# Performance work log

Hardware: AMD Instinct MI355X
Metric: run time of the kernel (lower is better)

The kernel has to match this reference:

```python
import jax, jax.numpy as jnp
import numpy as np

B, T, H, OUT = 16384, 128, 256, 10
EPS = 1e-5


def setup_inputs() -> dict:
    key = jax.random.key(0)
    ks = jax.random.split(key, 8)
    x = jax.random.randint(ks[0], (B, T, 1), 0, 10).astype(jnp.float32)
    def lin(k, fan_out, fan_in):
        bound = 1.0 / np.sqrt(fan_in)
        kw, kb = jax.random.split(k)
        w = jax.random.uniform(kw, (fan_out, fan_in), jnp.float32, -bound, bound)
        b = jax.random.uniform(kb, (fan_out,), jnp.float32, -bound, bound)
        return w, b
    embed_w, embed_b = lin(ks[1], H, 1)
    update_w, update_b = lin(ks[2], H, H)
    out_w, out_b = lin(ks[3], OUT, H)
    return {
        "x": x,
        "embed_w": embed_w, "embed_b": embed_b,
        "update_w": update_w, "update_b": update_b,
        "gamma": jnp.ones((H,), jnp.float32), "beta": jnp.zeros((H,), jnp.float32),
        "out_w": out_w, "out_b": out_b,
    }


def _layer_norm(h, gamma, beta):
    mu = jnp.mean(h, axis=-1, keepdims=True)
    var = jnp.mean(jnp.square(h - mu), axis=-1, keepdims=True)
    return (h - mu) * jax.lax.rsqrt(var + EPS) * gamma + beta


def reference(x, embed_w, embed_b, update_w, update_b, gamma, beta, out_w, out_b):
    # embed is per-timestep independent -> precompute for all T at once: [B,T,H]
    inp_all = jnp.tanh(jnp.einsum('bti,hi->bth', x, embed_w) + embed_b)

    def step(h, inp_t):  # h:[B,H], inp_t:[B,H]
        h = jnp.tanh((inp_t + h) @ update_w.T + update_b)
        h = _layer_norm(h, gamma, beta)
        return h, None

    h0 = jnp.zeros((x.shape[0], embed_w.shape[0]), x.dtype)
    h, _ = jax.lax.scan(step, h0, jnp.swapaxes(inp_all, 0, 1))  # scan over T
    return h @ out_w.T + out_b  # [B, 10]
```

## Files before the change

kernel.cpp:

```cpp
#include <hip/hip_runtime.h>
#include <hip/hip_fp16.h>
#include <math.h>

typedef _Float16 f16;
typedef _Float16 f16x2 __attribute__((ext_vector_type(2)));
typedef _Float16 f16x8 __attribute__((ext_vector_type(8)));
typedef float f32x4 __attribute__((ext_vector_type(4)));
typedef unsigned char u8;

#define HDIM 256
#define TST 128
#define OUTD 10
#define S2LE 2.8853900817779268f

static __device__ __forceinline__ f16x2 pkrtz(float a, float b) {
  auto r = __builtin_amdgcn_cvt_pkrtz(a, b);
  return *(f16x2*)&r;
}

__global__ __launch_bounds__(256, 2) void rnn_kernel(
    const float* __restrict__ x,
    const float* __restrict__ embed_w,
    const float* __restrict__ embed_b,
    const float* __restrict__ update_w,
    const float* __restrict__ update_b,
    const float* __restrict__ gamma,
    const float* __restrict__ beta,
    const float* __restrict__ out_w,
    const float* __restrict__ out_b,
    float* __restrict__ out)
{
  __shared__ __align__(16) f16   sFR[2][8][64][8];
  __shared__ __align__(16) float sD1[10 * 260];
  __shared__ __align__(16) float sBW[HDIM];
  __shared__ __align__(16) float sRSg[HDIM];
  __shared__ __align__(16) float sST[2][16][10][2];
  __shared__ float sOB[16];
  __shared__ u8    sXb[TST][32];

  const int tid = threadIdx.x;
  const int w  = tid >> 6;
  const int l  = tid & 63;
  const int q  = l >> 4;
  const int ml = l & 15;
  const int m3 = ml & 3;
  const int base = blockIdx.x * 32;
  const int nb = w * 64 + q * 4;
  const int diagw = (q == (ml >> 2));

  float* T0 = (float*)&sFR[0][0][0][0];

  {
    float ew = embed_w[tid], eb = embed_b[tid];
    #pragma unroll
    for (int xv = 0; xv < 10; xv++)
      T0[tid * 10 + xv] = tanhf((float)xv * ew + eb);
  }
  for (int idx = tid; idx < 32 * TST; idx += 256) {
    int col = idx >> 7, tt = idx & 127;
    sXb[tt][col] = (u8)(int)x[(size_t)(base + col) * TST + tt];
  }
  if (tid < 16) {
    float v = 0.f;
    if (tid < OUTD) {
      v = out_b[tid];
      const float* orow = out_w + tid * HDIM;
      for (int k = 0; k < HDIM; k += 4) {
        float4 wv = *(const float4*)(orow + k);
        float4 bv = *(const float4*)(beta + k);
        v = fmaf(wv.x, bv.x, fmaf(wv.y, bv.y, fmaf(wv.z, bv.z, fmaf(wv.w, bv.w, v))));
      }
    }
    sOB[tid] = v;
  }
  __syncthreads();

  {
    const int n = tid;
    const float* wrow = update_w + n * HDIM;
    float ty[10];
    #pragma unroll
    for (int xv = 0; xv < 10; xv++) ty[xv] = 0.f;
    float bw = 0.f, rsg = 0.f;
    for (int k = 0; k < HDIM; k += 4) {
      float4 wv4 = *(const float4*)(wrow + k);
      float4 b4  = *(const float4*)(beta + k);
      float4 g4  = *(const float4*)(gamma + k);
      bw  = fmaf(wv4.x, b4.x, fmaf(wv4.y, b4.y, fmaf(wv4.z, b4.z, fmaf(wv4.w, b4.w, bw))));
      rsg = fmaf(wv4.x, S2LE * g4.x, fmaf(wv4.y, S2LE * g4.y,
            fmaf(wv4.z, S2LE * g4.z, fmaf(wv4.w, S2LE * g4.w, rsg))));
      #pragma unroll
      for (int kk = 0; kk < 4; kk++) {
        float wv = ((const float*)&wv4)[kk];
        const float* t0r = T0 + (k + kk) * 10;
        #pragma unroll
        for (int xv = 0; xv < 10; xv++) ty[xv] = fmaf(wv, t0r[xv], ty[xv]);
      }
    }
    float ubn = update_b[n];
    sBW[n]  = S2LE * bw;
    sRSg[n] = rsg;
    #pragma unroll
    for (int xv = 0; xv < 10; xv++)
      sD1[xv * 260 + n] = S2LE * (ty[xv] + ubn + bw);
  }
  __syncthreads();

  f16x8 wf[4][8];
  #pragma unroll
  for (int c = 0; c < 8; c++) {
    const int k0 = c * 32 + q * 4;
    float4 g0 = *(const float4*)(gamma + k0);
    float4 g1 = *(const float4*)(gamma + k0 + 16);
    #pragma unroll
    for (int nt = 0; nt < 4; nt++) {
      const float* wrow = update_w + (w * 64 + nt * 16 + ml) * HDIM;
      float4 a0 = *(const float4*)(wrow + k0);
      float4 a1 = *(const float4*)(wrow + k0 + 16);
      f16x8 f;
      f[0]=(f16)(S2LE*g0.x*a0.x); f[1]=(f16)(S2LE*g0.y*a0.y);
      f[2]=(f16)(S2LE*g0.z*a0.z); f[3]=(f16)(S2LE*g0.w*a0.w);
      f[4]=(f16)(S2LE*g1.x*a1.x); f[5]=(f16)(S2LE*g1.y*a1.y);
      f[6]=(f16)(S2LE*g1.z*a1.z); f[7]=(f16)(S2LE*g1.w*a1.w);
      wf[nt][c] = f;
    }
  }
  f32x4 rsgr[4];
  #pragma unroll
  for (int nt = 0; nt < 4; nt++)
    rsgr[nt] = *(const f32x4*)(sRSg + nb + nt * 16);

  f16x8 ones_;
  #pragma unroll
  for (int j = 0; j < 8; j++) ones_[j] = (f16)1.f;
  const f32x4 zeros_ = {0.f, 0.f, 0.f, 0.f};

  f32x4 acc0[4], acc1[4];

  {
    #pragma unroll
    for (int g = 0; g < 2; g++) {
      const int xv0 = (int)sXb[0][g * 16 + ml];
      const float* dp = sD1 + xv0 * 260;
      #pragma unroll
      for (int cp = 0; cp < 2; cp++) {
        union { f16x8 v8; f16x2 v2[4]; } pk;
        #pragma unroll
        for (int h = 0; h < 2; h++) {
          const int nt = 2 * cp + h;
          f32x4 dd = *(const f32x4*)(dp + nb + nt * 16);
          f32x4 bw = *(const f32x4*)(sBW + nb + nt * 16);
          float tq[4];
          #pragma unroll
          for (int r = 0; r < 4; r++) {
            float y = dd[r] - bw[r];
            float e = __builtin_amdgcn_exp2f(y);
            float tv = fmaf(-2.f, __builtin_amdgcn_rcpf(e + 1.f), 1.f);
            tq[r] = tv;
          }
          pk.v2[2 * h]     = pkrtz(tq[0], tq[1]);
          pk.v2[2 * h + 1] = pkrtz(tq[2], tq[3]);
        }
        *(f16x8*)&sFR[g][2 * w + cp][l][0] = pk.v8;
      }
    }
    __syncthreads();
  }

#define MMG(FB, CC, CUR, NXT, ACC)                                             \
    { if ((CC) < 7) NXT = *(const f16x8*)((FB) + ((CC) + 1) * 512 + l * 8);    \
      ACC[0] = __builtin_amdgcn_mfma_f32_16x16x32_f16(wf[0][CC], CUR, ACC[0],0,0,0); \
      ACC[1] = __builtin_amdgcn_mfma_f32_16x16x32_f16(wf[1][CC], CUR, ACC[1],0,0,0); \
      ACC[2] = __builtin_amdgcn_mfma_f32_16x16x32_f16(wf[2][CC], CUR, ACC[2],0,0,0); \
      ACC[3] = __builtin_amdgcn_mfma_f32_16x16x32_f16(wf[3][CC], CUR, ACC[3],0,0,0); }

#define GSEL(AG, SEL)                                                          \
    { SEL = AG[0];                                                             \
      SEL = (m3 == 1) ? AG[1] : SEL;                                           \
      SEL = (m3 == 2) ? AG[2] : SEL;                                           \
      SEL = (m3 == 3) ? AG[3] : SEL; }

#define STATRD(G, S1, S2)                                                      \
    { const float* sp_ = &sST[G][ml][0][0];                                    \
      f32x4 a0_ = *(const f32x4*)(sp_);                                        \
      f32x4 a1_ = *(const f32x4*)(sp_ + 4);                                    \
      f32x4 a2_ = *(const f32x4*)(sp_ + 8);                                    \
      f32x4 a3_ = *(const f32x4*)(sp_ + 12);                                   \
      S1 = ((a0_[0] + a0_[2]) + (a1_[0] + a1_[2]))                             \
         + ((a2_[0] + a2_[2]) + (a3_[0] + a3_[2]));                            \
      S2 = ((a0_[1] + a0_[3]) + (a1_[1] + a1_[3]))                             \
         + ((a2_[1] + a2_[3]) + (a3_[1] + a3_[3])); }

#define STATOWN(FB, G)                                                         \
    { f16x8 ro0_ = *(const f16x8*)((FB) + (2 * w) * 512 + l * 8);              \
      f16x8 ro1_ = *(const f16x8*)((FB) + (2 * w + 1) * 512 + l * 8);          \
      f32x4 aG0_ = __builtin_amdgcn_mfma_f32_16x16x32_f16(ro0_, ro0_, zeros_,0,0,0); \
      f32x4 aS0_ = __builtin_amdgcn_mfma_f32_16x16x32_f16(ones_, ro0_, zeros_,0,0,0); \
      f32x4 aG1_ = __builtin_amdgcn_mfma_f32_16x16x32_f16(ro1_, ro1_, zeros_,0,0,0); \
      f32x4 aS1_ = __builtin_amdgcn_mfma_f32_16x16x32_f16(ones_, ro1_, zeros_,0,0,0); \
      float sel0_, sel1_;                                                      \
      GSEL(aG0_, sel0_)                                                        \
      GSEL(aG1_, sel1_)                                                        \
      if (diagw)                                                               \
        *(f32x4*)&sST[G][ml][2 * w][0] =                                       \
            (f32x4){aS0_[0], sel0_, aS1_[0], sel1_};                           \
    }

#define SLICE(S, ACCE)                                                         \
    { _Pragma("unroll") for (int r_ = 0; r_ < 4; r_++) {                       \
        float y_ = fmaf(rs_, ACCE[S][r_], fmaf(-rm_, rsgr[S][r_], dd_[S][r_]));\
        float e_ = __builtin_amdgcn_exp2f(y_);                                 \
        tv_[S][r_] = fmaf(-2.f, __builtin_amdgcn_rcpf(e_ + 1.f), 1.f); } }

#define PACK(GE, CP)                                                           \
    { union { f16x8 v8; f16x2 v2[4]; } k_;                                     \
      k_.v2[0] = pkrtz(tv_[2*(CP)][0],   tv_[2*(CP)][1]);                      \
      k_.v2[1] = pkrtz(tv_[2*(CP)][2],   tv_[2*(CP)][3]);                      \
      k_.v2[2] = pkrtz(tv_[2*(CP)+1][0], tv_[2*(CP)+1][1]);                    \
      k_.v2[3] = pkrtz(tv_[2*(CP)+1][2], tv_[2*(CP)+1][3]);                    \
      *(f16x8*)&sFR[GE][2 * w + (CP)][l][0] = k_.v8; }

#define PHASE(TE, GM, GE, XOFF, ACCM, ACCE)                                    \
  {                                                                            \
    float s1_, s2_;                                                            \
    STATRD(GE, s1_, s2_)                                                       \
    const int xv_ = (int)sXb[TE][XOFF + ml];                                   \
    const float* dp_ = sD1 + xv_ * 260 + nb;                                   \
    f32x4 dd_[4];                                                              \
    _Pragma("unroll") for (int n_ = 0; n_ < 4; n_++)                           \
      dd_[n_] = *(const f32x4*)(dp_ + n_ * 16);                                \
    const f16* fbm_ = &sFR[GM][0][0][0];                                       \
    f16x8 rA_ = *(const f16x8*)(fbm_ + l * 8);                                 \
    f16x8 rB_;                                                                 \
    f32x4 tv_[4];                                                              \
    __builtin_amdgcn_s_setprio(1);                                             \
    rB_ = *(const f16x8*)(fbm_ + 512 + l * 8);                                 \
    ACCM[0] = __builtin_amdgcn_mfma_f32_16x16x32_f16(wf[0][0], rA_, zeros_,0,0,0); \
    ACCM[1] = __builtin_amdgcn_mfma_f32_16x16x32_f16(wf[1][0], rA_, zeros_,0,0,0); \
    ACCM[2] = __builtin_amdgcn_mfma_f32_16x16x32_f16(wf[2][0], rA_, zeros_,0,0,0); \
    ACCM[3] = __builtin_amdgcn_mfma_f32_16x16x32_f16(wf[3][0], rA_, zeros_,0,0,0); \
    MMG(fbm_, 1, rB_, rA_, ACCM)                                               \
    float mu_ = s1_ * (1.f / 256.f);                                           \
    float rs_ = __frsqrt_rn(fmaf(s2_, 1.f / 256.f, -mu_ * mu_) + 1e-5f);       \
    float rm_ = rs_ * mu_;                                                     \
    SLICE(0, ACCE)                                                             \
    MMG(fbm_, 2, rA_, rB_, ACCM)                                               \
    MMG(fbm_, 3, rB_, rA_, ACCM)                                               \
    SLICE(1, ACCE)                                                             \
    PACK(GE, 0)                                                                \
    MMG(fbm_, 4, rA_, rB_, ACCM)                                               \
    MMG(fbm_, 5, rB_, rA_, ACCM)                                               \
    SLICE(2, ACCE)                                                             \
    MMG(fbm_, 6, rA_, rB_, ACCM)                                               \
    MMG(fbm_, 7, rB_, rA_, ACCM)                                               \
    SLICE(3, ACCE)                                                             \
    PACK(GE, 1)                                                                \
    STATOWN(fbm_, GM)                                                          \
    __builtin_amdgcn_s_setprio(0);                                             \
    __syncthreads();                                                           \
  }

  {
    const f16* fbm_ = &sFR[0][0][0][0];
    f16x8 rA_ = *(const f16x8*)(fbm_ + l * 8);
    f16x8 rB_;
    rB_ = *(const f16x8*)(fbm_ + 512 + l * 8);
    acc0[0] = __builtin_amdgcn_mfma_f32_16x16x32_f16(wf[0][0], rA_, zeros_,0,0,0);
    acc0[1] = __builtin_amdgcn_mfma_f32_16x16x32_f16(wf[1][0], rA_, zeros_,0,0,0);
    acc0[2] = __builtin_amdgcn_mfma_f32_16x16x32_f16(wf[2][0], rA_, zeros_,0,0,0);
    acc0[3] = __builtin_amdgcn_mfma_f32_16x16x32_f16(wf[3][0], rA_, zeros_,0,0,0);
    MMG(fbm_, 1, rB_, rA_, acc0)
    MMG(fbm_, 2, rA_, rB_, acc0)
    MMG(fbm_, 3, rB_, rA_, acc0)
    MMG(fbm_, 4, rA_, rB_, acc0)
    MMG(fbm_, 5, rB_, rA_, acc0)
    MMG(fbm_, 6, rA_, rB_, acc0)
    MMG(fbm_, 7, rB_, rA_, acc0)
    STATOWN(fbm_, 0)
    __syncthreads();
  }

  #pragma unroll 1
  for (int t = 1; t <= 127; t++) {
    PHASE(t, 1, 0, 0,  acc1, acc0)
    PHASE(t, 0, 1, 16, acc0, acc1)
  }

  {
    const f16* fb1 = &sFR[1][0][0][0];
    STATOWN(fb1, 1)
    f16x8 fin0[2], fin1[2];
    #pragma unroll
    for (int cp = 0; cp < 2; cp++) {
      fin0[cp] = *(const f16x8*)&sFR[0][2 * w + cp][l][0];
      fin1[cp] = *(const f16x8*)&sFR[1][2 * w + cp][l][0];
    }
    __syncthreads();

    float rsF[2], nmF[2];
    {
      float s1, s2;
      STATRD(0, s1, s2)
      float mu = s1 * (1.f / 256.f);
      float ve = fmaf(s2, 1.f / 256.f, -mu * mu) + 1e-5f;
      rsF[0] = __frsqrt_rn(ve); nmF[0] = -rsF[0] * mu;
      STATRD(1, s1, s2)
      mu = s1 * (1.f / 256.f);
      ve = fmaf(s2, 1.f / 256.f, -mu * mu) + 1e-5f;
      rsF[1] = __frsqrt_rn(ve); nmF[1] = -rsF[1] * mu;
    }

    f16* sOW = (f16*)sD1;
    for (int idx = tid; idx < 512; idx += 256) {
      int c = idx >> 6, l2 = idx & 63, q2 = l2 >> 4, o = l2 & 15;
      int k0 = c * 32 + q2 * 4;
      f16x8 f;
      #pragma unroll
      for (int j = 0; j < 8; j++) f[j] = (f16)0.f;
      if (o < OUTD) {
        const float* orow = out_w + o * HDIM;
        float4 a0 = *(const float4*)(orow + k0);
        float4 a1 = *(const float4*)(orow + k0 + 16);
        float4 g0 = *(const float4*)(gamma + k0);
        float4 g1 = *(const float4*)(gamma + k0 + 16);
        f[0]=(f16)(g0.x*a0.x); f[1]=(f16)(g0.y*a0.y); f[2]=(f16)(g0.z*a0.z); f[3]=(f16)(g0.w*a0.w);
        f[4]=(f16)(g1.x*a1.x); f[5]=(f16)(g1.y*a1.y); f[6]=(f16)(g1.z*a1.z); f[7]=(f16)(g1.w*a1.w);
      }
      *(f16x8*)(sOW + idx * 8) = f;
    }
    __syncthreads();

    float* sOut = (float*)&sFR[0][0][0][0];
    #pragma unroll
    for (int g = 0; g < 2; g++) {
      f32x4 aO = zeros_;
      #pragma unroll
      for (int cp = 0; cp < 2; cp++) {
        f16x8 fr = (g == 0) ? fin0[cp] : fin1[cp];
        f16x8 af;
        #pragma unroll
        for (int j = 0; j < 8; j++)
          af[j] = (f16)fmaf(rsF[g], (float)fr[j], nmF[g]);
        f16x8 of = *(const f16x8*)(sOW + ((size_t)(2 * w + cp) * 64 + l) * 8);
        aO = __builtin_amdgcn_mfma_f32_16x16x32_f16(of, af, aO, 0, 0, 0);
      }
      #pragma unroll
      for (int r = 0; r < 4; r++)
        sOut[((g * 4 + w) * 16 + ml) * 16 + q * 4 + r] = aO[r];
    }
    __syncthreads();
    for (int idx = tid; idx < 32 * OUTD; idx += 256) {
      int m = idx / OUTD, o = idx - m * OUTD;
      int g = m >> 4, mm = m & 15;
      float s = 0.f;
      #pragma unroll
      for (int ww = 0; ww < 4; ww++) s += sOut[((g * 4 + ww) * 16 + mm) * 16 + o];
      out[(size_t)(base + m) * OUTD + o] = s + sOB[o];
    }
  }
}

extern "C" void kernel_launch(void* const* d_in, const int* in_sizes, int n_in,
                              void* d_out, int out_size, void* d_ws, size_t ws_size,
                              hipStream_t stream) {
  const float* x   = (const float*)d_in[0];
  const float* ew  = (const float*)d_in[1];
  const float* eb  = (const float*)d_in[2];
  const float* uw  = (const float*)d_in[3];
  const float* ub  = (const float*)d_in[4];
  const float* g   = (const float*)d_in[5];
  const float* be  = (const float*)d_in[6];
  const float* ow  = (const float*)d_in[7];
  const float* ob  = (const float*)d_in[8];
  float* out = (float*)d_out;

  const int B = in_sizes[0] / TST;
  const int grid = B / 32;
  hipLaunchKernelGGL(rnn_kernel, dim3(grid), dim3(256), 0, stream,
                     x, ew, eb, uw, ub, g, be, ow, ob, out);
}
```

Measured before the change: 317.9 us.

## Prefetch next-step embed rows and hoist LN stat MFMAs to phase start

The per-phase embedding lookup (sD1 rows indexed by the next timestep's token) is now loaded one phase ahead into persistent ddA/ddB registers, so it leaves the critical path. The Gram/sum MFMAs that feed layer-norm statistics are issued at the start of each phase rather than at the end, and their reduction and store move to the tail. The s_setprio hints are removed and the last iteration is peeled out. This costs extra VGPRs for the prefetched rows and the early stat results, which may push register pressure against the 2-wave launch bound.

```diff
diff --git a/kernel.cpp b/kernel.cpp
--- a/kernel.cpp
+++ b/kernel.cpp
@@ -136,6 +136,7 @@
   const f32x4 zeros_ = {0.f, 0.f, 0.f, 0.f};
 
   f32x4 acc0[4], acc1[4];
+  f32x4 ddA[4], ddB[4];
 
   {
     #pragma unroll
@@ -206,9 +207,9 @@
             (f32x4){aS0_[0], sel0_, aS1_[0], sel1_};                           \
     }
 
-#define SLICE(S, ACCE)                                                         \
+#define SLICE(S, ACCE, DD)                                                     \
     { _Pragma("unroll") for (int r_ = 0; r_ < 4; r_++) {                       \
-        float y_ = fmaf(rs_, ACCE[S][r_], fmaf(-rm_, rsgr[S][r_], dd_[S][r_]));\
+        float y_ = fmaf(rs_, ACCE[S][r_], fmaf(-rm_, rsgr[S][r_], DD[S][r_])); \
         float e_ = __builtin_amdgcn_exp2f(y_);                                 \
         tv_[S][r_] = fmaf(-2.f, __builtin_amdgcn_rcpf(e_ + 1.f), 1.f); } }
 
@@ -220,20 +221,20 @@
       k_.v2[3] = pkrtz(tv_[2*(CP)+1][2], tv_[2*(CP)+1][3]);                    \
       *(f16x8*)&sFR[GE][2 * w + (CP)][l][0] = k_.v8; }
 
-#define PHASE(TE, GM, GE, XOFF, ACCM, ACCE)                                    \
+#define PHASE(TE, TN, GM, GE, XOFF, ACCM, ACCE, DD)                            \
   {                                                                            \
+    const f16* fbm_ = &sFR[GM][0][0][0];                                       \
+    f16x8 ro0_ = *(const f16x8*)(fbm_ + (2 * w) * 512 + l * 8);                \
+    f16x8 ro1_ = *(const f16x8*)(fbm_ + (2 * w + 1) * 512 + l * 8);            \
+    f32x4 aG0_ = __builtin_amdgcn_mfma_f32_16x16x32_f16(ro0_, ro0_, zeros_,0,0,0); \
+    f32x4 aS0_ = __builtin_amdgcn_mfma_f32_16x16x32_f16(ones_, ro0_, zeros_,0,0,0); \
+    f32x4 aG1_ = __builtin_amdgcn_mfma_f32_16x16x32_f16(ro1_, ro1_, zeros_,0,0,0); \
+    f32x4 aS1_ = __builtin_amdgcn_mfma_f32_16x16x32_f16(ones_, ro1_, zeros_,0,0,0); \
     float s1_, s2_;                                                            \
     STATRD(GE, s1_, s2_)                                                       \
-    const int xv_ = (int)sXb[TE][XOFF + ml];                                   \
-    const float* dp_ = sD1 + xv_ * 260 + nb;                                   \
-    f32x4 dd_[4];                                                              \
-    _Pragma("unroll") for (int n_ = 0; n_ < 4; n_++)                           \
-      dd_[n_] = *(const f32x4*)(dp_ + n_ * 16);                                \
-    const f16* fbm_ = &sFR[GM][0][0][0];                                       \
     f16x8 rA_ = *(const f16x8*)(fbm_ + l * 8);                                 \
     f16x8 rB_;                                                                 \
     f32x4 tv_[4];                                                              \
-    __builtin_amdgcn_s_setprio(1);                                             \
     rB_ = *(const f16x8*)(fbm_ + 512 + l * 8);                                 \
     ACCM[0] = __builtin_amdgcn_mfma_f32_16x16x32_f16(wf[0][0], rA_, zeros_,0,0,0); \
     ACCM[1] = __builtin_amdgcn_mfma_f32_16x16x32_f16(wf[1][0], rA_, zeros_,0,0,0); \
@@ -243,20 +244,32 @@
     float mu_ = s1_ * (1.f / 256.f);                                           \
     float rs_ = __frsqrt_rn(fmaf(s2_, 1.f / 256.f, -mu_ * mu_) + 1e-5f);       \
     float rm_ = rs_ * mu_;                                                     \
-    SLICE(0, ACCE)                                                             \
+    SLICE(0, ACCE, DD)                                                         \
     MMG(fbm_, 2, rA_, rB_, ACCM)                                               \
     MMG(fbm_, 3, rB_, rA_, ACCM)                                               \
-    SLICE(1, ACCE)                                                             \
+    SLICE(1, ACCE, DD)                                                         \
     PACK(GE, 0)                                                                \
     MMG(fbm_, 4, rA_, rB_, ACCM)                                               \
     MMG(fbm_, 5, rB_, rA_, ACCM)                                               \
-    SLICE(2, ACCE)                                                             \
+    SLICE(2, ACCE, DD)                                                         \
     MMG(fbm_, 6, rA_, rB_, ACCM)                                               \
     MMG(fbm_, 7, rB_, rA_, ACCM)                                               \
-    SLICE(3, ACCE)                                                             \
+    SLICE(3, ACCE, DD)                                                         \
     PACK(GE, 1)                                                                \
-    STATOWN(fbm_, GM)                                                          \
-    __builtin_amdgcn_s_setprio(0);                                             \
+    {                                                                          \
+      const int xvn_ = (int)sXb[TN][XOFF + ml];                                \
+      const float* dpn_ = sD1 + xvn_ * 260 + nb;                               \
+      _Pragma("unroll") for (int n_ = 0; n_ < 4; n_++)                         \
+        DD[n_] = *(const f32x4*)(dpn_ + n_ * 16);                              \
+    }                                                                          \
+    {                                                                          \
+      float sel0_, sel1_;                                                      \
+      GSEL(aG0_, sel0_)                                                        \
+      GSEL(aG1_, sel1_)                                                        \
+      if (diagw)                                                               \
+        *(f32x4*)&sST[GM][ml][2 * w][0] =                                      \
+            (f32x4){aS0_[0], sel0_, aS1_[0], sel1_};                           \
+    }                                                                          \
     __syncthreads();                                                           \
   }
 
@@ -277,14 +290,27 @@
     MMG(fbm_, 6, rA_, rB_, acc0)
     MMG(fbm_, 7, rB_, rA_, acc0)
     STATOWN(fbm_, 0)
+    {
+      const int xva = (int)sXb[1][ml];
+      const float* dpa = sD1 + xva * 260 + nb;
+      const int xvb = (int)sXb[1][16 + ml];
+      const float* dpb = sD1 + xvb * 260 + nb;
+      #pragma unroll
+      for (int n_ = 0; n_ < 4; n_++) {
+        ddA[n_] = *(const f32x4*)(dpa + n_ * 16);
+        ddB[n_] = *(const f32x4*)(dpb + n_ * 16);
+      }
+    }
     __syncthreads();
   }
 
   #pragma unroll 1
-  for (int t = 1; t <= 127; t++) {
-    PHASE(t, 1, 0, 0,  acc1, acc0)
-    PHASE(t, 0, 1, 16, acc0, acc1)
-  }
+  for (int t = 1; t <= 126; t++) {
+    PHASE(t, t + 1, 1, 0, 0,  acc1, acc0, ddA)
+    PHASE(t, t + 1, 0, 1, 16, acc0, acc1, ddB)
+  }
+  PHASE(127, 127, 1, 0, 0,  acc1, acc0, ddA)
+  PHASE(127, 127, 0, 1, 16, acc0, acc1, ddB)
 
   {
     const f16* fb1 = &sFR[1][0][0][0];
```

Result: slower. 381.8 us (+20.1%).
